# Kernel optimization log

Measured on AMD Instinct MI355X. Metric: run time of the kernel, lower is better.

Reference implementation:

```python
import jax, jax.numpy as jnp
import numpy as np


def setup_inputs() -> dict:
    key = jax.random.key(0)
    ks = jax.random.split(key, 8)
    H = 256  # hidden_size
    NH = 8   # num_heads
    HD = H // NH
    B, G = 256, 1024
    s = 1.0 / np.sqrt(H)
    return {
        "query": jax.random.normal(ks[0], (B, 2 * H), dtype=jnp.float32),
        "ref": jax.random.normal(ks[1], (B, G, H), dtype=jnp.float32),
        "Wq": jax.random.normal(ks[2], (H, 2 * H), dtype=jnp.float32) * s,
        "bq": jax.random.normal(ks[3], (H,), dtype=jnp.float32) * s,
        "We": jax.random.normal(ks[4], (H, H), dtype=jnp.float32) * s,
        "be": jax.random.normal(ks[5], (H,), dtype=jnp.float32) * s,
        "Wv": jax.random.normal(ks[6], (HD,), dtype=jnp.float32) * (1.0 / np.sqrt(HD)),
        "bv": jax.random.normal(ks[7], (1,), dtype=jnp.float32) * 0.01,
        "num_heads": 8,
    }


def reference(query, ref, Wq, bq, We, be, Wv, bv, num_heads):
    B, G, H = ref.shape
    hd = H // num_heads
    # q_dense: [B, 2H] -> [B, H] -> [B, nh, hd]
    q = (query @ Wq.T + bq).reshape(B, num_heads, hd)
    # e_dense: [B, G, H] -> [B, G, H] -> [B, G, nh, hd]
    e = (jnp.einsum('bgh,oh->bgo', ref, We) + be).reshape(B, G, num_heads, hd)
    # broadcast-add over graph dim, tanh, per-head linear scorer (hd -> 1)
    v = jnp.tanh(q[:, None, :, :] + e)                 # [B, G, nh, hd]
    s = jnp.einsum('bgnd,d->bgn', v, Wv) + bv[0]       # [B, G, nh]
    # sum over heads, output [B, 1, G] (matches sum(dim=1).transpose(1,2))
    return s.sum(axis=-1)[:, None, :]
```

## Files before the change

kernel.cpp:

```cpp
#include <hip/hip_runtime.h>

typedef __attribute__((ext_vector_type(8))) short short8;
typedef __attribute__((ext_vector_type(8))) unsigned short ushort8;
typedef __attribute__((ext_vector_type(4))) float f32x4;
typedef unsigned short ushort;
typedef unsigned int uint;

__device__ __forceinline__ ushort f2bf(float f) {
    uint x = __float_as_uint(f);
    x += 0x7fffu + ((x >> 16) & 1u);
    return (ushort)(x >> 16);
}

__device__ __forceinline__ uint pack2bf(float x, float y) {
    uint xi = __float_as_uint(x) + 0x8000u;
    uint yi = __float_as_uint(y) + 0x8000u;
    return __builtin_amdgcn_perm(yi, xi, 0x07060302u);
}

__global__ __launch_bounds__(256) void prep(
    const float* __restrict__ query, const float* __restrict__ Wq,
    const float* __restrict__ bq, const float* __restrict__ be,
    const float* __restrict__ We, float* __restrict__ q_ws,
    ushort* __restrict__ Web) {
    __shared__ float qrow[512];
    const int t = threadIdx.x;
    if (blockIdx.x < 64) {
        const int i = (blockIdx.x * 256 + t) * 4;
        float4 v = *(const float4*)(We + i);
        ushort4 u;
        u.x = f2bf(v.x); u.y = f2bf(v.y); u.z = f2bf(v.z); u.w = f2bf(v.w);
        *(ushort4*)(Web + i) = u;
        return;
    }
    const int b = blockIdx.x - 64;
    qrow[t]       = query[b * 512 + t];
    qrow[t + 256] = query[b * 512 + 256 + t];
    __syncthreads();
    const f32x4* wr = (const f32x4*)(Wq + (size_t)t * 512);
    float s0 = 0.f, s1 = 0.f, s2 = 0.f, s3 = 0.f;
#pragma unroll 4
    for (int j = 0; j < 128; j += 4) {
        f32x4 w0 = wr[j], w1 = wr[j + 1], w2 = wr[j + 2], w3 = wr[j + 3];
        f32x4 q0 = *(const f32x4*)(qrow + 4 * j);
        f32x4 q1 = *(const f32x4*)(qrow + 4 * j + 4);
        f32x4 q2 = *(const f32x4*)(qrow + 4 * j + 8);
        f32x4 q3 = *(const f32x4*)(qrow + 4 * j + 12);
        s0 += w0.x * q0.x + w0.y * q0.y + w0.z * q0.z + w0.w * q0.w;
        s1 += w1.x * q1.x + w1.y * q1.y + w1.z * q1.z + w1.w * q1.w;
        s2 += w2.x * q2.x + w2.y * q2.y + w2.z * q2.z + w2.w * q2.w;
        s3 += w3.x * q3.x + w3.y * q3.y + w3.z * q3.z + w3.w * q3.w;
    }
    q_ws[b * 256 + t] = (s0 + s1) + (s2 + s3) + bq[t] + be[t];
}

#define BM 64
#define LDA 264

__global__ __launch_bounds__(256, 3) void fused_gemm(
    const float* __restrict__ ref, const ushort* __restrict__ Web,
    const float* __restrict__ q_ws, const float* __restrict__ Wv,
    const float* __restrict__ bv, float* __restrict__ out) {
    __shared__ ushort Asm[BM * LDA];
    __shared__ float red[4][64];

    const int t = threadIdx.x;
    const int w = t >> 6;
    const int l = t & 63;
    const int quad = l >> 4;
    const int lr = l & 15;
    const size_t row0 = (size_t)blockIdx.x * BM;
    const int b = (int)(row0 >> 10);

    const ushort* Bp = Web + ((size_t)(w * 64 + lr)) * 256 + quad * 8;
    short8 bcur[4];
#pragma unroll
    for (int cb = 0; cb < 4; ++cb)
        bcur[cb] = *(const short8*)(Bp + cb * 16 * 256);

    {
        const int row = t >> 2;
        const int colbase = (t & 3) * 64;
        const float4* ap = (const float4*)(ref + (row0 + row) * 256 + colbase);
        uint* as = (uint*)(Asm + row * LDA + colbase);
#pragma unroll
        for (int c = 0; c < 2; ++c) {
            float4 buf[8];
#pragma unroll
            for (int j = 0; j < 8; ++j) buf[j] = ap[c * 8 + j];
#pragma unroll
            for (int j = 0; j < 4; ++j) {
                float4 x = buf[2 * j], y = buf[2 * j + 1];
                uint4 p;
                p.x = pack2bf(x.x, x.y);
                p.y = pack2bf(x.z, x.w);
                p.z = pack2bf(y.x, y.y);
                p.w = pack2bf(y.z, y.w);
                *(uint4*)(as + c * 16 + j * 4) = p;
            }
        }
    }

    const float* qe = q_ws + b * 256;
    const float wv0 = Wv[lr];
    const float wv1 = Wv[16 + lr];
    const float bvv = bv[0];
    float qv[4];
#pragma unroll
    for (int cb = 0; cb < 4; ++cb) qv[cb] = qe[w * 64 + cb * 16 + lr];

    __syncthreads();

    f32x4 acc[4][4];
#pragma unroll
    for (int i = 0; i < 4; ++i)
#pragma unroll
        for (int j = 0; j < 4; ++j) acc[i][j] = (f32x4){0.f, 0.f, 0.f, 0.f};

    const ushort* Ap = Asm + lr * LDA + quad * 8;
#pragma unroll
    for (int k = 0; k < 8; ++k) {
        short8 bnxt[4];
        if (k < 7) {
#pragma unroll
            for (int cb = 0; cb < 4; ++cb)
                bnxt[cb] = *(const short8*)(Bp + cb * 16 * 256 + (k + 1) * 32);
        }
        short8 afr[4];
#pragma unroll
        for (int rb = 0; rb < 4; ++rb)
            afr[rb] = *(const short8*)(Ap + rb * 16 * LDA + k * 32);
#pragma unroll
        for (int rb = 0; rb < 4; ++rb)
#pragma unroll
            for (int cb = 0; cb < 4; ++cb)
                acc[rb][cb] = __builtin_amdgcn_mfma_f32_16x16x32_bf16(
                    afr[rb], bcur[cb], acc[rb][cb], 0, 0, 0);
        if (k < 7) {
#pragma unroll
            for (int cb = 0; cb < 4; ++cb) bcur[cb] = bnxt[cb];
        }
    }

    float part[4][4];
#pragma unroll
    for (int rb = 0; rb < 4; ++rb)
#pragma unroll
        for (int r = 0; r < 4; ++r) part[rb][r] = 0.f;

#pragma unroll
    for (int cb = 0; cb < 4; ++cb) {
        const float wvv = (cb & 1) ? wv1 : wv0;
#pragma unroll
        for (int rb = 0; rb < 4; ++rb)
#pragma unroll
            for (int r = 0; r < 4; ++r) {
                float x = acc[rb][cb][r] + qv[cb];
                float th = 1.f - 2.f / (__expf(2.f * x) + 1.f);
                part[rb][r] += th * wvv;
            }
    }
#pragma unroll
    for (int off = 1; off < 16; off <<= 1)
#pragma unroll
        for (int rb = 0; rb < 4; ++rb)
#pragma unroll
            for (int r = 0; r < 4; ++r)
                part[rb][r] += __shfl_xor(part[rb][r], off, 64);

    if (lr == 0) {
#pragma unroll
        for (int rb = 0; rb < 4; ++rb)
#pragma unroll
            for (int r = 0; r < 4; ++r)
                red[w][rb * 16 + quad * 4 + r] = part[rb][r];
    }
    __syncthreads();
    if (t < 64) {
        float s = red[0][t] + red[1][t] + red[2][t] + red[3][t] + 8.f * bvv;
        out[row0 + t] = s;
    }
}

extern "C" void kernel_launch(void* const* d_in, const int* in_sizes, int n_in,
                              void* d_out, int out_size, void* d_ws, size_t ws_size,
                              hipStream_t stream) {
    const float* query = (const float*)d_in[0];
    const float* ref   = (const float*)d_in[1];
    const float* Wq    = (const float*)d_in[2];
    const float* bq    = (const float*)d_in[3];
    const float* We    = (const float*)d_in[4];
    const float* be    = (const float*)d_in[5];
    const float* Wv    = (const float*)d_in[6];
    const float* bv    = (const float*)d_in[7];
    float* out = (float*)d_out;

    float*  q_ws = (float*)d_ws;
    ushort* Web  = (ushort*)((char*)d_ws + 65536 * sizeof(float));

    prep<<<320, 256, 0, stream>>>(query, Wq, bq, be, We, q_ws, Web);
    fused_gemm<<<4096, 256, 0, stream>>>(ref, Web, q_ws, Wv, bv, out);
}
```

Baseline: 444.1 us.

## Store A tile in fragment-ordered LDS layout and simplify tanh epilogue algebra

```diff
diff --git a/kernel.cpp b/kernel.cpp
--- a/kernel.cpp
+++ b/kernel.cpp
@@ -6,6 +6,21 @@
 typedef unsigned short ushort;
 typedef unsigned int uint;
 
+__device__ __forceinline__ float fast_exp2(float x) {
+#if __has_builtin(__builtin_amdgcn_exp2f)
+    return __builtin_amdgcn_exp2f(x);
+#else
+    return __expf(x * 0.6931471805599453f);
+#endif
+}
+__device__ __forceinline__ float fast_rcp(float x) {
+#if __has_builtin(__builtin_amdgcn_rcpf)
+    return __builtin_amdgcn_rcpf(x);
+#else
+    return __frcp_rn(x);
+#endif
+}
+
 __device__ __forceinline__ ushort f2bf(float f) {
     uint x = __float_as_uint(f);
     x += 0x7fffu + ((x >> 16) & 1u);
@@ -21,8 +36,9 @@
 __global__ __launch_bounds__(256) void prep(
     const float* __restrict__ query, const float* __restrict__ Wq,
     const float* __restrict__ bq, const float* __restrict__ be,
-    const float* __restrict__ We, float* __restrict__ q_ws,
-    ushort* __restrict__ Web) {
+    const float* __restrict__ We, const float* __restrict__ Wv,
+    const float* __restrict__ bv, float* __restrict__ q_ws,
+    ushort* __restrict__ Web, float* __restrict__ aux) {
     __shared__ float qrow[512];
     const int t = threadIdx.x;
     if (blockIdx.x < 64) {
@@ -31,6 +47,14 @@
         ushort4 u;
         u.x = f2bf(v.x); u.y = f2bf(v.y); u.z = f2bf(v.z); u.w = f2bf(v.w);
         *(ushort4*)(Web + i) = u;
+        return;
+    }
+    if (blockIdx.x == 320) {
+        if (t >= 64) return;
+        float v = (t < 32) ? Wv[t] : 0.f;
+#pragma unroll
+        for (int off = 1; off < 32; off <<= 1) v += __shfl_xor(v, off, 64);
+        if (t == 0) aux[0] = 8.f * (v + bv[0]);
         return;
     }
     const int b = blockIdx.x - 64;
@@ -55,13 +79,12 @@
 }
 
 #define BM 64
-#define LDA 264
-
-__global__ __launch_bounds__(256, 3) void fused_gemm(
+
+__global__ __launch_bounds__(256, 4) void fused_gemm(
     const float* __restrict__ ref, const ushort* __restrict__ Web,
     const float* __restrict__ q_ws, const float* __restrict__ Wv,
-    const float* __restrict__ bv, float* __restrict__ out) {
-    __shared__ ushort Asm[BM * LDA];
+    const float* __restrict__ aux, float* __restrict__ out) {
+    __shared__ uint4 Asm[2048];
     __shared__ float red[4][64];
 
     const int t = threadIdx.x;
@@ -72,42 +95,41 @@
     const size_t row0 = (size_t)blockIdx.x * BM;
     const int b = (int)(row0 >> 10);
 
+    {
+        const float* ap = ref + (row0 + w * 16 + lr) * 256 + quad * 8;
+#pragma unroll
+        for (int half = 0; half < 2; ++half) {
+            float4 f[8];
+#pragma unroll
+            for (int kb = 0; kb < 4; ++kb) {
+                f[2 * kb]     = *(const float4*)(ap + (half * 4 + kb) * 32);
+                f[2 * kb + 1] = *(const float4*)(ap + (half * 4 + kb) * 32 + 4);
+            }
+#pragma unroll
+            for (int kb = 0; kb < 4; ++kb) {
+                uint4 p;
+                p.x = pack2bf(f[2 * kb].x,     f[2 * kb].y);
+                p.y = pack2bf(f[2 * kb].z,     f[2 * kb].w);
+                p.z = pack2bf(f[2 * kb + 1].x, f[2 * kb + 1].y);
+                p.w = pack2bf(f[2 * kb + 1].z, f[2 * kb + 1].w);
+                Asm[(w * 8 + half * 4 + kb) * 64 + l] = p;
+            }
+        }
+    }
+
     const ushort* Bp = Web + ((size_t)(w * 64 + lr)) * 256 + quad * 8;
     short8 bcur[4];
 #pragma unroll
     for (int cb = 0; cb < 4; ++cb)
         bcur[cb] = *(const short8*)(Bp + cb * 16 * 256);
 
-    {
-        const int row = t >> 2;
-        const int colbase = (t & 3) * 64;
-        const float4* ap = (const float4*)(ref + (row0 + row) * 256 + colbase);
-        uint* as = (uint*)(Asm + row * LDA + colbase);
-#pragma unroll
-        for (int c = 0; c < 2; ++c) {
-            float4 buf[8];
-#pragma unroll
-            for (int j = 0; j < 8; ++j) buf[j] = ap[c * 8 + j];
-#pragma unroll
-            for (int j = 0; j < 4; ++j) {
-                float4 x = buf[2 * j], y = buf[2 * j + 1];
-                uint4 p;
-                p.x = pack2bf(x.x, x.y);
-                p.y = pack2bf(x.z, x.w);
-                p.z = pack2bf(y.x, y.y);
-                p.w = pack2bf(y.z, y.w);
-                *(uint4*)(as + c * 16 + j * 4) = p;
-            }
-        }
-    }
-
+    const float c2l = 2.885390081777927f;
     const float* qe = q_ws + b * 256;
-    const float wv0 = Wv[lr];
-    const float wv1 = Wv[16 + lr];
-    const float bvv = bv[0];
-    float qv[4];
-#pragma unroll
-    for (int cb = 0; cb < 4; ++cb) qv[cb] = qe[w * 64 + cb * 16 + lr];
+    const float w2a = -2.f * Wv[lr];
+    const float w2b = -2.f * Wv[16 + lr];
+    float qvc[4];
+#pragma unroll
+    for (int cb = 0; cb < 4; ++cb) qvc[cb] = qe[w * 64 + cb * 16 + lr] * c2l;
 
     __syncthreads();
 
@@ -117,7 +139,7 @@
 #pragma unroll
         for (int j = 0; j < 4; ++j) acc[i][j] = (f32x4){0.f, 0.f, 0.f, 0.f};
 
-    const ushort* Ap = Asm + lr * LDA + quad * 8;
+    const ushort* As = (const ushort*)Asm;
 #pragma unroll
     for (int k = 0; k < 8; ++k) {
         short8 bnxt[4];
@@ -129,7 +151,7 @@
         short8 afr[4];
 #pragma unroll
         for (int rb = 0; rb < 4; ++rb)
-            afr[rb] = *(const short8*)(Ap + rb * 16 * LDA + k * 32);
+            afr[rb] = *(const short8*)(As + ((rb * 8 + k) * 64 + l) * 8);
 #pragma unroll
         for (int rb = 0; rb < 4; ++rb)
 #pragma unroll
@@ -150,14 +172,13 @@
 
 #pragma unroll
     for (int cb = 0; cb < 4; ++cb) {
-        const float wvv = (cb & 1) ? wv1 : wv0;
+        const float w2 = (cb & 1) ? w2b : w2a;
 #pragma unroll
         for (int rb = 0; rb < 4; ++rb)
 #pragma unroll
             for (int r = 0; r < 4; ++r) {
-                float x = acc[rb][cb][r] + qv[cb];
-                float th = 1.f - 2.f / (__expf(2.f * x) + 1.f);
-                part[rb][r] += th * wvv;
+                float e = fast_exp2(fmaf(acc[rb][cb][r], c2l, qvc[cb]));
+                part[rb][r] = fmaf(w2, fast_rcp(e + 1.f), part[rb][r]);
             }
     }
 #pragma unroll
@@ -177,7 +198,7 @@
     }
     __syncthreads();
     if (t < 64) {
-        float s = red[0][t] + red[1][t] + red[2][t] + red[3][t] + 8.f * bvv;
+        float s = red[0][t] + red[1][t] + red[2][t] + red[3][t] + aux[0];
         out[row0 + t] = s;
     }
 }
@@ -196,8 +217,9 @@
     float* out = (float*)d_out;
 
     float*  q_ws = (float*)d_ws;
-    ushort* Web  = (ushort*)((char*)d_ws + 65536 * sizeof(float));
-
-    prep<<<320, 256, 0, stream>>>(query, Wq, bq, be, We, q_ws, Web);
-    fused_gemm<<<4096, 256, 0, stream>>>(ref, Web, q_ws, Wv, bv, out);
-}
+    ushort* Web  = (ushort*)((char*)d_ws + 262144);
+    float*  aux  = (float*)((char*)d_ws + 262144 + 131072);
+
+    prep<<<321, 256, 0, stream>>>(query, Wq, bq, be, We, Wv, bv, q_ws, Web, aux);
+    fused_gemm<<<4096, 256, 0, stream>>>(ref, Web, q_ws, Wv, aux, out);
+}
```

After: 419.4 us. 1.06x faster.
